# Kernel tuning notes

Hardware: AMD Instinct MI355X
Metric: run time of the kernel (lower is better)

The kernel has to match this reference:

```python
import jax, jax.numpy as jnp
import numpy as np

N, T, D, H = 32, 2048, 256, 256


def setup_inputs() -> dict:
    key = jax.random.key(0)
    k0, k1, k2, k3, k4 = jax.random.split(key, 5)
    std = 1.0 / np.sqrt(H + D)  # matches PTLSTM.reset()
    return {
        "x": jax.random.normal(k0, (N, T, D), dtype=jnp.float32),
        "state": jnp.zeros((N, 2 * H), dtype=jnp.float32),  # [h0 | c0]
        "w_ih": (jax.random.normal(k1, (4 * H, D)) * std).astype(jnp.float32),
        "w_hh": (jax.random.normal(k2, (4 * H, H)) * std).astype(jnp.float32),
        "b_ih": (jax.random.normal(k3, (4 * H,)) * std).astype(jnp.float32),
        "b_hh": (jax.random.normal(k4, (4 * H,)) * std).astype(jnp.float32),
    }


def reference(x, state, w_ih, w_hh, b_ih, b_hh):
    # Single-layer batch_first LSTM, PyTorch gate order (i, f, g, o).
    Hd = w_hh.shape[1]
    h0, c0 = state[:, :Hd], state[:, Hd:]
    # Precompute input-to-hidden projection for all timesteps (one big GEMM).
    xg = jnp.einsum('ntd,gd->ntg', x, w_ih) + (b_ih + b_hh)  # [N, T, 4H]

    def step(carry, xg_t):
        h, c = carry
        gates = xg_t + h @ w_hh.T  # [N, 4H]
        i, f, g, o = jnp.split(gates, 4, axis=-1)
        i = jax.nn.sigmoid(i)
        f = jax.nn.sigmoid(f)
        g = jnp.tanh(g)
        o = jax.nn.sigmoid(o)
        c = f * c + i * g
        h = o * jnp.tanh(c)
        return (h, c), h

    (hT, cT), out_t = jax.lax.scan(step, (h0, c0), jnp.swapaxes(xg, 0, 1))
    output = jnp.swapaxes(out_t, 0, 1)  # [N, T, H]
    outstate = jnp.concatenate([hT, cT], axis=1)  # [N, 2H]
    return output, outstate
```

## Files before the change

kernel.cpp:

```cpp
#include <hip/hip_runtime.h>

typedef _Float16 half2_t __attribute__((ext_vector_type(2)));
typedef __bf16   bf16x8  __attribute__((ext_vector_type(8)));
typedef float    f32x4   __attribute__((ext_vector_type(4)));
typedef unsigned short u16x8 __attribute__((ext_vector_type(8)));
typedef unsigned int  uint32;
typedef unsigned long long uint64;

#define LSTM_N 32
#define LSTM_T 2048
#define LSTM_D 256
#define LSTM_H 256
#define NG 1024
#define CH 256
#define NCH (LSTM_T / CH)
#define MCH (LSTM_N * CH)

#define OFF_XG   ((size_t)0)
#define SZ_XG    ((size_t)MCH * NG * 4)
#define OFF_WIHB (OFF_XG + SZ_XG)
#define SZ_WIHB  ((size_t)NG * LSTM_D * 2)
#define OFF_BIAS (OFF_WIHB + SZ_WIHB)
#define SZ_BIAS  ((size_t)4096)
#define OFF_WPK  (OFF_BIAS + SZ_BIAS)
#define SZ_WPK   ((size_t)2 * 512 * 128 * 4)
#define OFF_CST  (OFF_WPK + SZ_WPK)
#define SZ_CST   ((size_t)LSTM_N * 256 * 4)
#define OFF_HST  (OFF_CST + SZ_CST)
#define SZ_HST   ((size_t)LSTM_N * 128 * 4)
#define OFF_HX   (OFF_HST + SZ_HST)
#define SZ_HX    ((size_t)LSTM_N * 2 * 2 * 64 * 8)

#if defined(__has_builtin)
#if __has_builtin(__builtin_amdgcn_fdot2)
#define HAVE_FDOT2 1
#endif
#endif

__device__ __forceinline__ float fdot2(uint32 w, uint32 h, float acc) {
#ifdef HAVE_FDOT2
  return __builtin_amdgcn_fdot2(__builtin_bit_cast(half2_t, w),
                                __builtin_bit_cast(half2_t, h), acc, false);
#else
  half2_t wv = __builtin_bit_cast(half2_t, w);
  half2_t hv = __builtin_bit_cast(half2_t, h);
  float r = fmaf((float)wv.x, (float)hv.x, acc);
  return fmaf((float)wv.y, (float)hv.y, r);
#endif
}

__device__ __forceinline__ float sigm(float x) { return 1.f / (1.f + __expf(-x)); }
__device__ __forceinline__ float tanh_fast(float x) { return 2.f / (1.f + __expf(-2.f * x)) - 1.f; }

__device__ __forceinline__ unsigned short f2bf(float f) {
  uint32 u = __builtin_bit_cast(uint32, f);
  uint32 r = (u + 0x7FFFu + ((u >> 16) & 1u)) >> 16;
  return (unsigned short)r;
}

__device__ __forceinline__ float bfly8(const float a[8], int kap) {
  float k0[4], g0[4];
  const bool b4 = (kap & 4) != 0;
#pragma unroll
  for (int v = 0; v < 4; ++v) {
    k0[v] = b4 ? a[v + 4] : a[v];
    g0[v] = b4 ? a[v] : a[v + 4];
  }
#pragma unroll
  for (int v = 0; v < 4; ++v) k0[v] += __shfl_xor(g0[v], 4, 64);
  float k1[2], g1[2];
  const bool b2 = (kap & 2) != 0;
#pragma unroll
  for (int v = 0; v < 2; ++v) {
    k1[v] = b2 ? k0[v + 2] : k0[v];
    g1[v] = b2 ? k0[v] : k0[v + 2];
  }
#pragma unroll
  for (int v = 0; v < 2; ++v) k1[v] += __shfl_xor(g1[v], 2, 64);
  const bool b1 = (kap & 1) != 0;
  float k2 = b1 ? k1[1] : k1[0];
  float g2 = b1 ? k1[0] : k1[1];
  return k2 + __shfl_xor(g2, 1, 64);
}


__global__ void cvt_bf16_k(const float* __restrict__ src, unsigned short* __restrict__ dst, int n) {
  int i = blockIdx.x * blockDim.x + threadIdx.x;
  if (4 * i + 3 < n) {
    float4 v = ((const float4*)src)[i];
    ushort4 o;
    o.x = f2bf(v.x); o.y = f2bf(v.y); o.z = f2bf(v.z); o.w = f2bf(v.w);
    ((ushort4*)dst)[i] = o;
  }
}

__global__ void bias_sum_k(const float* __restrict__ bih, const float* __restrict__ bhh,
                           float* __restrict__ bias) {
  int g = blockIdx.x * blockDim.x + threadIdx.x;
  if (g < NG) bias[g] = bih[g] + bhh[g];
}

__global__ void wpack_k(const float* __restrict__ whh, uint32* __restrict__ wpk) {
  int e = blockIdx.x * blockDim.x + threadIdx.x;
  int p = e >> 16;
  int i128 = (e >> 9) & 127;
  int t = e & 511;
  int j = i128 >> 4, m = i128 & 15;
  int w = t >> 6, l = t & 63;
  int q = l >> 4, b3 = (l >> 3) & 1, kap = l & 7;
  int row = q * 256 + 128 * p + 16 * w + 8 * b3 + j;
  int k = (m < 8) ? (128 * p + 16 * kap + 2 * m)
                  : (128 * (1 - p) + 16 * kap + 2 * (m - 8));
  half2_t h;
  h.x = (_Float16)whh[row * 256 + k];
  h.y = (_Float16)whh[row * 256 + k + 1];
  wpk[((i128 >> 2) * 1024 + p * 512 + t) * 4 + (i128 & 3)] = __builtin_bit_cast(uint32, h);
}

__global__ void state_init_k(const float* __restrict__ state, float* __restrict__ cst,
                             uint32* __restrict__ hst, uint64* __restrict__ hx) {
  int i = blockIdx.x * blockDim.x + threadIdx.x;
  int n = i >> 8, j = i & 255;
  cst[i] = state[n * 512 + 256 + j];
  if ((j & 1) == 0) {
    half2_t h2;
    h2.x = (_Float16)state[n * 512 + j];
    h2.y = (_Float16)state[n * 512 + j + 1];
    hst[(n << 7) + (j >> 1)] = __builtin_bit_cast(uint32, h2);
  }
  hx[i] = 0ull;
}

__global__ __launch_bounds__(256) void gemm_xg(const float* __restrict__ x,
                                               const unsigned short* __restrict__ wb,
                                               const float* __restrict__ bias,
                                               float* __restrict__ xg, int ch) {
  __shared__ unsigned short As[128 * 40];
  __shared__ unsigned short Bs[128 * 40];
  const int tid = threadIdx.x;
  const int m0 = blockIdx.y * 128;
  const int g0 = blockIdx.x * 128;
  const int w = tid >> 6;
  const int lane = tid & 63;
  const int wm = (w >> 1) * 64, wn = (w & 1) * 64;
  const int row_l = tid >> 2;
  const int q = tid & 3;
  const int lr = lane & 15, kg = lane >> 4;

  size_t grow[2];
#pragma unroll
  for (int r = 0; r < 2; ++r) {
    int gm = m0 + row_l + 64 * r;
    grow[r] = (size_t)(gm >> 8) * LSTM_T + (size_t)ch * CH + (gm & 255);
  }

  f32x4 acc[4][4];
#pragma unroll
  for (int i = 0; i < 4; ++i)
#pragma unroll
    for (int j = 0; j < 4; ++j) acc[i][j] = (f32x4){0.f, 0.f, 0.f, 0.f};

  for (int kt = 0; kt < 8; ++kt) {
#pragma unroll
    for (int r = 0; r < 2; ++r) {
      int row = row_l + 64 * r;
      const float* ap = x + grow[r] * 256 + kt * 32 + q * 8;
      float4 v0 = *(const float4*)ap;
      float4 v1 = *(const float4*)(ap + 4);
      u16x8 o;
      o[0] = f2bf(v0.x); o[1] = f2bf(v0.y); o[2] = f2bf(v0.z); o[3] = f2bf(v0.w);
      o[4] = f2bf(v1.x); o[5] = f2bf(v1.y); o[6] = f2bf(v1.z); o[7] = f2bf(v1.w);
      *(uint4*)((char*)As + row * 80 + q * 16) = __builtin_bit_cast(uint4, o);
      uint4 bv = *(const uint4*)(wb + (size_t)(g0 + row) * 256 + kt * 32 + q * 8);
      *(uint4*)((char*)Bs + row * 80 + q * 16) = bv;
    }
    __syncthreads();
    bf16x8 af[4], bfr[4];
#pragma unroll
    for (int i = 0; i < 4; ++i)
      af[i] = __builtin_bit_cast(bf16x8, *(const uint4*)((char*)As + (wm + 16 * i + lr) * 80 + kg * 16));
#pragma unroll
    for (int j = 0; j < 4; ++j)
      bfr[j] = __builtin_bit_cast(bf16x8, *(const uint4*)((char*)Bs + (wn + 16 * j + lr) * 80 + kg * 16));
#pragma unroll
    for (int i = 0; i < 4; ++i)
#pragma unroll
      for (int j = 0; j < 4; ++j)
        acc[i][j] = __builtin_amdgcn_mfma_f32_16x16x32_bf16(af[i], bfr[j], acc[i][j], 0, 0, 0);
    __syncthreads();
  }
#pragma unroll
  for (int j = 0; j < 4; ++j) {
    int gc = g0 + wn + 16 * j + lr;
    float bj = bias[gc];
#pragma unroll
    for (int i = 0; i < 4; ++i) {
#pragma unroll
      for (int r = 0; r < 4; ++r) {
        int m = m0 + wm + 16 * i + kg * 4 + r;
        xg[(size_t)m * NG + gc] = acc[i][j][r] + bj;
      }
    }
  }
}

__global__ __launch_bounds__(512, 1) void lstm_scan(const float* __restrict__ xg,
                                                    const uint4* __restrict__ wpk4,
                                                    float* __restrict__ cst,
                                                    uint32* __restrict__ hst,
                                                    uint64* __restrict__ hx,
                                                    float* __restrict__ out, int ch) {
  __shared__ uint32 hown[2][64];
  __shared__ uint32 hpeer[64];
  __shared__ float ostage[16][128];

  const int b = blockIdx.x;
  const int n = b & 31;
  const int p = b >> 5;
  const int t = threadIdx.x;
  const int w = t >> 6, l = t & 63;
  const int q = l >> 4, kap = l & 7;
  const int u = 16 * w + (l & 15);
  const int R = q * 256 + 128 * p + u;

  uint32 wr[128];
#pragma unroll
  for (int ig = 0; ig < 32; ++ig) {
    uint4 v = wpk4[ig * 1024 + p * 512 + t];
    wr[4 * ig + 0] = v.x; wr[4 * ig + 1] = v.y; wr[4 * ig + 2] = v.z; wr[4 * ig + 3] = v.w;
  }
  float c = cst[n * 256 + 128 * p + u];
  if (t < 64) {
    hown[0][t] = hst[n * 128 + 64 * p + t];
    hpeer[t]   = hst[n * 128 + 64 * (1 - p) + t];
  }
  __syncthreads();

  const float* xgn = xg + (size_t)n * CH * NG;
  float* outb = out + ((size_t)n * LSTM_T + (size_t)ch * CH) * LSTM_H;
  uint64* hx_own  = hx + (size_t)(n * 2 + p) * 128;
  uint64* hx_peer = hx + (size_t)(n * 2 + (1 - p)) * 128;
  const int gsbase = ch * CH;

  float xcur = xgn[R];

  for (int tt = 0; tt < CH; ++tt) {
    const uint32 gs = (uint32)(gsbase + tt);
    float xnext = (tt < CH - 1) ? xgn[(size_t)(tt + 1) * NG + R] : 0.f;
    uint32 hro[8];
    *(uint4*)&hro[0] = *(const uint4*)&hown[tt & 1][8 * kap];
    *(uint4*)&hro[4] = *(const uint4*)&hown[tt & 1][8 * kap + 4];
    float acc[8];
#pragma unroll
    for (int j = 0; j < 8; ++j) {
      float a = 0.f;
#pragma unroll
      for (int m = 0; m < 8; ++m) a = fdot2(wr[j * 16 + m], hro[m], a);
      acc[j] = a;
    }
    if (tt > 0 && t < 64) {
      uint64 v;
      do {
        v = __hip_atomic_load(&hx_peer[(size_t)(tt & 1) * 64 + t],
                              __ATOMIC_RELAXED, __HIP_MEMORY_SCOPE_AGENT);
      } while ((uint32)(v >> 32) != gs);
      hpeer[t] = (uint32)v;
    }
    __syncthreads();
    uint32 hrp[8];
    *(uint4*)&hrp[0] = *(const uint4*)&hpeer[8 * kap];
    *(uint4*)&hrp[4] = *(const uint4*)&hpeer[8 * kap + 4];
#pragma unroll
    for (int j = 0; j < 8; ++j) {
      float a = acc[j];
#pragma unroll
      for (int m = 0; m < 8; ++m) a = fdot2(wr[j * 16 + 8 + m], hrp[m], a);
      acc[j] = a;
    }
    float s = bfly8(acc, kap);
    float pre = s + xcur;
    xcur = xnext;
    float z = (q == 2) ? (2.f * pre) : pre;
    float sg = 1.f / (1.f + __expf(-z));
    float a_own = (q == 2) ? (2.f * sg - 1.f) : sg;
    float a1 = __shfl_xor(a_own, 16, 64);
    float a2 = __shfl_xor(a_own, 32, 64);
    float a3 = __shfl_xor(a1, 32, 64);
    float gi = (q == 0) ? a_own : ((q == 1) ? a1 : ((q == 2) ? a2 : a3));
    float gf = (q == 1) ? a_own : ((q == 0) ? a1 : ((q == 3) ? a2 : a3));
    float gg = (q == 2) ? a_own : ((q == 3) ? a1 : ((q == 0) ? a2 : a3));
    float go = (q == 3) ? a_own : ((q == 2) ? a1 : ((q == 1) ? a2 : a3));
    c = gf * c + gi * gg;
    float h = go * tanh_fast(c);
    _Float16 hf16 = (_Float16)h;
    uint32 hz = (uint32)__builtin_bit_cast(unsigned short, hf16);
    uint32 hn = (uint32)__shfl_xor((int)hz, 1, 64);
    if (q == 0) {
      ((unsigned short*)&hown[(tt + 1) & 1][0])[u] = (unsigned short)hz;
      ostage[tt & 15][u] = h;
      if (tt < CH - 1 && (l & 1) == 0) {
        uint64 msg = (uint64)(hz | (hn << 16)) | ((uint64)(gs + 1) << 32);
        __hip_atomic_store(&hx_own[(size_t)((tt + 1) & 1) * 64 + (u >> 1)], msg,
                           __ATOMIC_RELAXED, __HIP_MEMORY_SCOPE_AGENT);
      }
      if (ch == NCH - 1 && tt == CH - 1) {
        float* os = out + (size_t)LSTM_N * LSTM_T * LSTM_H + n * 512;
        os[128 * p + u] = h;
        os[256 + 128 * p + u] = c;
      }
    }
    __syncthreads();
    if ((tt & 15) == 15) {
      int sl = t >> 5, q4 = t & 31;
      float4 v = *(const float4*)&ostage[sl][4 * q4];
      *(float4*)&outb[(size_t)(tt - 15 + sl) * LSTM_H + 128 * p + 4 * q4] = v;
    }
  }
  if (q == 0) cst[n * 256 + 128 * p + u] = c;
  if (t < 64) hst[n * 128 + 64 * p + t] = hown[0][t];
}

extern "C" void kernel_launch(void* const* d_in, const int* in_sizes, int n_in,
                              void* d_out, int out_size, void* d_ws, size_t ws_size,
                              hipStream_t stream) {
  const float* x   = (const float*)d_in[0];
  const float* st  = (const float*)d_in[1];
  const float* wih = (const float*)d_in[2];
  const float* whh = (const float*)d_in[3];
  const float* bih = (const float*)d_in[4];
  const float* bhh = (const float*)d_in[5];
  float* out = (float*)d_out;
  char* ws = (char*)d_ws;

  float* xg = (float*)(ws + OFF_XG);
  unsigned short* wihb = (unsigned short*)(ws + OFF_WIHB);
  float* bias = (float*)(ws + OFF_BIAS);
  uint32* wpk = (uint32*)(ws + OFF_WPK);
  float* cst = (float*)(ws + OFF_CST);
  uint32* hst = (uint32*)(ws + OFF_HST);
  uint64* hx = (uint64*)(ws + OFF_HX);

  cvt_bf16_k<<<(NG * LSTM_D / 4 + 255) / 256, 256, 0, stream>>>(wih, wihb, NG * LSTM_D);
  bias_sum_k<<<4, 256, 0, stream>>>(bih, bhh, bias);
  wpack_k<<<512, 256, 0, stream>>>(whh, wpk);
  state_init_k<<<32, 256, 0, stream>>>(st, cst, hst, hx);

  for (int ch = 0; ch < NCH; ++ch) {
    gemm_xg<<<dim3(NG / 128, MCH / 128), 256, 0, stream>>>(x, wihb, bias, xg, ch);
    lstm_scan<<<64, 512, 0, stream>>>(xg, (const uint4*)wpk, cst, hst, hx, out, ch);
  }
}
```

Before: 2.978 ms.

## Split recurrent matvec by K-halves and exchange partial gate sums instead of h

Each of the two blocks per sequence now multiplies all 1024 gate rows against only its own half of h, so no block waits for the peer's h before starting its matvec. Partial pre-activations for the peer's rows go through global memory slots tagged with a step counter. The owning block waits for them, applies the activations into shared memory, and updates the cell. This removes the bfly8 shuffle reduction and the mid-step wait on peer h. In exchange, each step sends 1024 64-bit messages per sequence instead of 64 and polls them with s_sleep.

```diff
diff --git a/kernel.cpp b/kernel.cpp
--- a/kernel.cpp
+++ b/kernel.cpp
@@ -28,8 +28,8 @@
 #define SZ_CST   ((size_t)LSTM_N * 256 * 4)
 #define OFF_HST  (OFF_CST + SZ_CST)
 #define SZ_HST   ((size_t)LSTM_N * 128 * 4)
-#define OFF_HX   (OFF_HST + SZ_HST)
-#define SZ_HX    ((size_t)LSTM_N * 2 * 2 * 64 * 8)
+#define OFF_HPX  (OFF_HST + SZ_HST)
+#define SZ_HPX   ((size_t)LSTM_N * 2 * 1024 * 8)
 
 #if defined(__has_builtin)
 #if __has_builtin(__builtin_amdgcn_fdot2)
@@ -58,31 +58,6 @@
   return (unsigned short)r;
 }
 
-__device__ __forceinline__ float bfly8(const float a[8], int kap) {
-  float k0[4], g0[4];
-  const bool b4 = (kap & 4) != 0;
-#pragma unroll
-  for (int v = 0; v < 4; ++v) {
-    k0[v] = b4 ? a[v + 4] : a[v];
-    g0[v] = b4 ? a[v] : a[v + 4];
-  }
-#pragma unroll
-  for (int v = 0; v < 4; ++v) k0[v] += __shfl_xor(g0[v], 4, 64);
-  float k1[2], g1[2];
-  const bool b2 = (kap & 2) != 0;
-#pragma unroll
-  for (int v = 0; v < 2; ++v) {
-    k1[v] = b2 ? k0[v + 2] : k0[v];
-    g1[v] = b2 ? k0[v] : k0[v + 2];
-  }
-#pragma unroll
-  for (int v = 0; v < 2; ++v) k1[v] += __shfl_xor(g1[v], 2, 64);
-  const bool b1 = (kap & 1) != 0;
-  float k2 = b1 ? k1[1] : k1[0];
-  float g2 = b1 ? k1[0] : k1[1];
-  return k2 + __shfl_xor(g2, 1, 64);
-}
-
 
 __global__ void cvt_bf16_k(const float* __restrict__ src, unsigned short* __restrict__ dst, int n) {
   int i = blockIdx.x * blockDim.x + threadIdx.x;
@@ -103,22 +78,19 @@
 __global__ void wpack_k(const float* __restrict__ whh, uint32* __restrict__ wpk) {
   int e = blockIdx.x * blockDim.x + threadIdx.x;
   int p = e >> 16;
-  int i128 = (e >> 9) & 127;
+  int i = (e >> 9) & 127;
   int t = e & 511;
-  int j = i128 >> 4, m = i128 & 15;
-  int w = t >> 6, l = t & 63;
-  int q = l >> 4, b3 = (l >> 3) & 1, kap = l & 7;
-  int row = q * 256 + 128 * p + 16 * w + 8 * b3 + j;
-  int k = (m < 8) ? (128 * p + 16 * kap + 2 * m)
-                  : (128 * (1 - p) + 16 * kap + 2 * (m - 8));
+  int rh = i >> 6, jj = i & 63;
+  int row = t + rh * 512;
+  int k = 128 * p + 2 * jj;
   half2_t h;
   h.x = (_Float16)whh[row * 256 + k];
   h.y = (_Float16)whh[row * 256 + k + 1];
-  wpk[((i128 >> 2) * 1024 + p * 512 + t) * 4 + (i128 & 3)] = __builtin_bit_cast(uint32, h);
+  wpk[((i >> 2) * 1024 + p * 512 + t) * 4 + (i & 3)] = __builtin_bit_cast(uint32, h);
 }
 
 __global__ void state_init_k(const float* __restrict__ state, float* __restrict__ cst,
-                             uint32* __restrict__ hst, uint64* __restrict__ hx) {
+                             uint32* __restrict__ hst, uint64* __restrict__ hpx) {
   int i = blockIdx.x * blockDim.x + threadIdx.x;
   int n = i >> 8, j = i & 255;
   cst[i] = state[n * 512 + 256 + j];
@@ -128,7 +100,8 @@
     h2.y = (_Float16)state[n * 512 + j + 1];
     hst[(n << 7) + (j >> 1)] = __builtin_bit_cast(uint32, h2);
   }
-  hx[i] = 0ull;
+#pragma unroll
+  for (int z = 0; z < 8; ++z) hpx[(size_t)i * 8 + z] = 0ull;
 }
 
 __global__ __launch_bounds__(256) void gemm_xg(const float* __restrict__ x,
@@ -208,101 +181,105 @@
                                                     const uint4* __restrict__ wpk4,
                                                     float* __restrict__ cst,
                                                     uint32* __restrict__ hst,
-                                                    uint64* __restrict__ hx,
+                                                    uint64* __restrict__ hpx,
                                                     float* __restrict__ out, int ch) {
+  __shared__ float actb[512];
   __shared__ uint32 hown[2][64];
-  __shared__ uint32 hpeer[64];
   __shared__ float ostage[16][128];
 
   const int b = blockIdx.x;
   const int n = b & 31;
   const int p = b >> 5;
   const int t = threadIdx.x;
-  const int w = t >> 6, l = t & 63;
-  const int q = l >> 4, kap = l & 7;
-  const int u = 16 * w + (l & 15);
-  const int R = q * 256 + 128 * p + u;
+  const int q1 = t >> 8;
+  const int v = t & 255;
+  const int u = v & 127;
+  const bool own = ((v >> 7) == p);
+  const bool iscell = own && (q1 == 0);
+  const int r1 = t, r2 = t + 512;
 
   uint32 wr[128];
 #pragma unroll
   for (int ig = 0; ig < 32; ++ig) {
-    uint4 v = wpk4[ig * 1024 + p * 512 + t];
-    wr[4 * ig + 0] = v.x; wr[4 * ig + 1] = v.y; wr[4 * ig + 2] = v.z; wr[4 * ig + 3] = v.w;
-  }
-  float c = cst[n * 256 + 128 * p + u];
-  if (t < 64) {
-    hown[0][t] = hst[n * 128 + 64 * p + t];
-    hpeer[t]   = hst[n * 128 + 64 * (1 - p) + t];
-  }
+    uint4 w4 = wpk4[ig * 1024 + p * 512 + t];
+    wr[4 * ig + 0] = w4.x; wr[4 * ig + 1] = w4.y; wr[4 * ig + 2] = w4.z; wr[4 * ig + 3] = w4.w;
+  }
+  float c = 0.f;
+  if (iscell) c = cst[n * 256 + 128 * p + u];
+  if (t < 64) hown[0][t] = hst[n * 128 + 64 * p + t];
   __syncthreads();
 
   const float* xgn = xg + (size_t)n * CH * NG;
   float* outb = out + ((size_t)n * LSTM_T + (size_t)ch * CH) * LSTM_H;
-  uint64* hx_own  = hx + (size_t)(n * 2 + p) * 128;
-  uint64* hx_peer = hx + (size_t)(n * 2 + (1 - p)) * 128;
+  uint64* slots = hpx + (size_t)n * 2048;
   const int gsbase = ch * CH;
 
-  float xcur = xgn[R];
+  float x1 = 0.f, x2 = 0.f;
+  if (own) { x1 = xgn[r1]; x2 = xgn[r2]; }
 
   for (int tt = 0; tt < CH; ++tt) {
-    const uint32 gs = (uint32)(gsbase + tt);
-    float xnext = (tt < CH - 1) ? xgn[(size_t)(tt + 1) * NG + R] : 0.f;
-    uint32 hro[8];
-    *(uint4*)&hro[0] = *(const uint4*)&hown[tt & 1][8 * kap];
-    *(uint4*)&hro[4] = *(const uint4*)&hown[tt & 1][8 * kap + 4];
-    float acc[8];
-#pragma unroll
-    for (int j = 0; j < 8; ++j) {
-      float a = 0.f;
-#pragma unroll
-      for (int m = 0; m < 8; ++m) a = fdot2(wr[j * 16 + m], hro[m], a);
-      acc[j] = a;
-    }
-    if (tt > 0 && t < 64) {
-      uint64 v;
-      do {
-        v = __hip_atomic_load(&hx_peer[(size_t)(tt & 1) * 64 + t],
-                              __ATOMIC_RELAXED, __HIP_MEMORY_SCOPE_AGENT);
-      } while ((uint32)(v >> 32) != gs);
-      hpeer[t] = (uint32)v;
+    const uint32 want = (uint32)(gsbase + tt) + 1;
+    const int par = tt & 1;
+    float a1 = 0.f, a2 = 0.f;
+    const uint32* hp = &hown[par][0];
+#pragma unroll
+    for (int c4 = 0; c4 < 4; ++c4) {
+      uint32 hh[16];
+      *(uint4*)&hh[0]  = *(const uint4*)&hp[16 * c4 + 0];
+      *(uint4*)&hh[4]  = *(const uint4*)&hp[16 * c4 + 4];
+      *(uint4*)&hh[8]  = *(const uint4*)&hp[16 * c4 + 8];
+      *(uint4*)&hh[12] = *(const uint4*)&hp[16 * c4 + 12];
+      float s1 = 0.f, s2 = 0.f;
+#pragma unroll
+      for (int j = 0; j < 16; ++j) {
+        s1 = fdot2(wr[16 * c4 + j],      hh[j], s1);
+        s2 = fdot2(wr[64 + 16 * c4 + j], hh[j], s2);
+      }
+      a1 += s1; a2 += s2;
+    }
+    if (own) {
+      uint64 m1, m2;
+      uint64* s1p = &slots[(size_t)par * 1024 + r1];
+      uint64* s2p = &slots[(size_t)par * 1024 + r2];
+      for (;;) {
+        m1 = __hip_atomic_load(s1p, __ATOMIC_RELAXED, __HIP_MEMORY_SCOPE_AGENT);
+        if ((uint32)(m1 >> 32) == want) break;
+        __builtin_amdgcn_s_sleep(1);
+      }
+      for (;;) {
+        m2 = __hip_atomic_load(s2p, __ATOMIC_RELAXED, __HIP_MEMORY_SCOPE_AGENT);
+        if ((uint32)(m2 >> 32) == want) break;
+        __builtin_amdgcn_s_sleep(1);
+      }
+      float pre1 = a1 + __builtin_bit_cast(float, (uint32)m1) + x1;
+      float pre2 = a2 + __builtin_bit_cast(float, (uint32)m2) + x2;
+      if (tt < CH - 1) {
+        x1 = xgn[(size_t)(tt + 1) * NG + r1];
+        x2 = xgn[(size_t)(tt + 1) * NG + r2];
+      }
+      float g1 = sigm(pre1);
+      float g2 = (q1 == 0) ? tanh_fast(pre2) : sigm(pre2);
+      actb[q1 * 128 + u] = g1;
+      actb[(q1 + 2) * 128 + u] = g2;
+    } else {
+      __hip_atomic_store(&slots[(size_t)par * 1024 + r1],
+                         (uint64)__builtin_bit_cast(uint32, a1) | ((uint64)want << 32),
+                         __ATOMIC_RELAXED, __HIP_MEMORY_SCOPE_AGENT);
+      __hip_atomic_store(&slots[(size_t)par * 1024 + r2],
+                         (uint64)__builtin_bit_cast(uint32, a2) | ((uint64)want << 32),
+                         __ATOMIC_RELAXED, __HIP_MEMORY_SCOPE_AGENT);
     }
     __syncthreads();
-    uint32 hrp[8];
-    *(uint4*)&hrp[0] = *(const uint4*)&hpeer[8 * kap];
-    *(uint4*)&hrp[4] = *(const uint4*)&hpeer[8 * kap + 4];
-#pragma unroll
-    for (int j = 0; j < 8; ++j) {
-      float a = acc[j];
-#pragma unroll
-      for (int m = 0; m < 8; ++m) a = fdot2(wr[j * 16 + 8 + m], hrp[m], a);
-      acc[j] = a;
-    }
-    float s = bfly8(acc, kap);
-    float pre = s + xcur;
-    xcur = xnext;
-    float z = (q == 2) ? (2.f * pre) : pre;
-    float sg = 1.f / (1.f + __expf(-z));
-    float a_own = (q == 2) ? (2.f * sg - 1.f) : sg;
-    float a1 = __shfl_xor(a_own, 16, 64);
-    float a2 = __shfl_xor(a_own, 32, 64);
-    float a3 = __shfl_xor(a1, 32, 64);
-    float gi = (q == 0) ? a_own : ((q == 1) ? a1 : ((q == 2) ? a2 : a3));
-    float gf = (q == 1) ? a_own : ((q == 0) ? a1 : ((q == 3) ? a2 : a3));
-    float gg = (q == 2) ? a_own : ((q == 3) ? a1 : ((q == 0) ? a2 : a3));
-    float go = (q == 3) ? a_own : ((q == 2) ? a1 : ((q == 1) ? a2 : a3));
-    c = gf * c + gi * gg;
-    float h = go * tanh_fast(c);
-    _Float16 hf16 = (_Float16)h;
-    uint32 hz = (uint32)__builtin_bit_cast(unsigned short, hf16);
-    uint32 hn = (uint32)__shfl_xor((int)hz, 1, 64);
-    if (q == 0) {
-      ((unsigned short*)&hown[(tt + 1) & 1][0])[u] = (unsigned short)hz;
+    if (iscell) {
+      float gi = actb[u];
+      float gf = actb[128 + u];
+      float gg = actb[256 + u];
+      float go = actb[384 + u];
+      c = gf * c + gi * gg;
+      float h = go * tanh_fast(c);
+      _Float16 hf = (_Float16)h;
+      ((unsigned short*)&hown[par ^ 1][0])[u] = __builtin_bit_cast(unsigned short, hf);
       ostage[tt & 15][u] = h;
-      if (tt < CH - 1 && (l & 1) == 0) {
-        uint64 msg = (uint64)(hz | (hn << 16)) | ((uint64)(gs + 1) << 32);
-        __hip_atomic_store(&hx_own[(size_t)((tt + 1) & 1) * 64 + (u >> 1)], msg,
-                           __ATOMIC_RELAXED, __HIP_MEMORY_SCOPE_AGENT);
-      }
       if (ch == NCH - 1 && tt == CH - 1) {
         float* os = out + (size_t)LSTM_N * LSTM_T * LSTM_H + n * 512;
         os[128 * p + u] = h;
@@ -312,11 +289,11 @@
     __syncthreads();
     if ((tt & 15) == 15) {
       int sl = t >> 5, q4 = t & 31;
-      float4 v = *(const float4*)&ostage[sl][4 * q4];
-      *(float4*)&outb[(size_t)(tt - 15 + sl) * LSTM_H + 128 * p + 4 * q4] = v;
-    }
-  }
-  if (q == 0) cst[n * 256 + 128 * p + u] = c;
+      float4 vv = *(const float4*)&ostage[sl][4 * q4];
+      *(float4*)&outb[(size_t)(tt - 15 + sl) * LSTM_H + 128 * p + 4 * q4] = vv;
+    }
+  }
+  if (iscell) cst[n * 256 + 128 * p + u] = c;
   if (t < 64) hst[n * 128 + 64 * p + t] = hown[0][t];
 }
 
@@ -338,15 +315,15 @@
   uint32* wpk = (uint32*)(ws + OFF_WPK);
   float* cst = (float*)(ws + OFF_CST);
   uint32* hst = (uint32*)(ws + OFF_HST);
-  uint64* hx = (uint64*)(ws + OFF_HX);
+  uint64* hpx = (uint64*)(ws + OFF_HPX);
 
   cvt_bf16_k<<<(NG * LSTM_D / 4 + 255) / 256, 256, 0, stream>>>(wih, wihb, NG * LSTM_D);
   bias_sum_k<<<4, 256, 0, stream>>>(bih, bhh, bias);
   wpack_k<<<512, 256, 0, stream>>>(whh, wpk);
-  state_init_k<<<32, 256, 0, stream>>>(st, cst, hst, hx);
+  state_init_k<<<32, 256, 0, stream>>>(st, cst, hst, hpx);
 
   for (int ch = 0; ch < NCH; ++ch) {
     gemm_xg<<<dim3(NG / 128, MCH / 128), 256, 0, stream>>>(x, wihb, bias, xg, ch);
-    lstm_scan<<<64, 512, 0, stream>>>(xg, (const uint4*)wpk, cst, hst, hx, out, ch);
-  }
-}
+    lstm_scan<<<64, 512, 0, stream>>>(xg, (const uint4*)wpk, cst, hst, hpx, out, ch);
+  }
+}
```

Measured after the change: 4.142 ms. 39.1% more time.

## Interleave two batch rows per scan block to hide peer h-exchange latency

Applied to the files above, without the earlier changes.

Each lstm_scan block now processes two batch rows (n and n+16) back to back within every timestep. Each row has its own shared h buffers, cell state and cross-block handshake, and the grid shrinks from 64 to 32 blocks. The aim is to hide the spin-wait on the peer block's hidden-state message for one row behind the recurrent matvec of the other row. It also drops one barrier per row-step. The cost is twice the serial work per block and fewer active CUs, so the critical path may simply get longer if the exchange latency is not the dominant cost.

```diff
diff --git a/kernel.cpp b/kernel.cpp
--- a/kernel.cpp
+++ b/kernel.cpp
@@ -49,7 +49,6 @@
 #endif
 }
 
-__device__ __forceinline__ float sigm(float x) { return 1.f / (1.f + __expf(-x)); }
 __device__ __forceinline__ float tanh_fast(float x) { return 2.f / (1.f + __expf(-2.f * x)) - 1.f; }
 
 __device__ __forceinline__ unsigned short f2bf(float f) {
@@ -210,13 +209,14 @@
                                                     uint32* __restrict__ hst,
                                                     uint64* __restrict__ hx,
                                                     float* __restrict__ out, int ch) {
-  __shared__ uint32 hown[2][64];
-  __shared__ uint32 hpeer[64];
-  __shared__ float ostage[16][128];
+  __shared__ uint32 hownA[2][64], hownB[2][64];
+  __shared__ uint32 hpeerA[64], hpeerB[64];
+  __shared__ float ostage[2][16][128];
 
   const int b = blockIdx.x;
-  const int n = b & 31;
-  const int p = b >> 5;
+  const int n = b & 15;
+  const int p = b >> 4;
+  const int nA = n, nB = n + 16;
   const int t = threadIdx.x;
   const int w = t >> 6, l = t & 63;
   const int q = l >> 4, kap = l & 7;
@@ -229,95 +229,179 @@
     uint4 v = wpk4[ig * 1024 + p * 512 + t];
     wr[4 * ig + 0] = v.x; wr[4 * ig + 1] = v.y; wr[4 * ig + 2] = v.z; wr[4 * ig + 3] = v.w;
   }
-  float c = cst[n * 256 + 128 * p + u];
+  float cA = cst[nA * 256 + 128 * p + u];
+  float cB = cst[nB * 256 + 128 * p + u];
   if (t < 64) {
-    hown[0][t] = hst[n * 128 + 64 * p + t];
-    hpeer[t]   = hst[n * 128 + 64 * (1 - p) + t];
+    hownA[0][t] = hst[nA * 128 + 64 * p + t];
+    hpeerA[t]   = hst[nA * 128 + 64 * (1 - p) + t];
+    hownB[0][t] = hst[nB * 128 + 64 * p + t];
+    hpeerB[t]   = hst[nB * 128 + 64 * (1 - p) + t];
   }
   __syncthreads();
 
-  const float* xgn = xg + (size_t)n * CH * NG;
-  float* outb = out + ((size_t)n * LSTM_T + (size_t)ch * CH) * LSTM_H;
-  uint64* hx_own  = hx + (size_t)(n * 2 + p) * 128;
-  uint64* hx_peer = hx + (size_t)(n * 2 + (1 - p)) * 128;
+  const float* xgA = xg + (size_t)nA * CH * NG;
+  const float* xgB = xg + (size_t)nB * CH * NG;
+  float* outA = out + ((size_t)nA * LSTM_T + (size_t)ch * CH) * LSTM_H;
+  float* outB = out + ((size_t)nB * LSTM_T + (size_t)ch * CH) * LSTM_H;
+  uint64* hxA_own  = hx + (size_t)(nA * 2 + p) * 128;
+  uint64* hxA_peer = hx + (size_t)(nA * 2 + (1 - p)) * 128;
+  uint64* hxB_own  = hx + (size_t)(nB * 2 + p) * 128;
+  uint64* hxB_peer = hx + (size_t)(nB * 2 + (1 - p)) * 128;
   const int gsbase = ch * CH;
 
-  float xcur = xgn[R];
+  float xcA = xgA[R];
+  float xcB = xgB[R];
 
   for (int tt = 0; tt < CH; ++tt) {
     const uint32 gs = (uint32)(gsbase + tt);
-    float xnext = (tt < CH - 1) ? xgn[(size_t)(tt + 1) * NG + R] : 0.f;
-    uint32 hro[8];
-    *(uint4*)&hro[0] = *(const uint4*)&hown[tt & 1][8 * kap];
-    *(uint4*)&hro[4] = *(const uint4*)&hown[tt & 1][8 * kap + 4];
-    float acc[8];
-#pragma unroll
-    for (int j = 0; j < 8; ++j) {
-      float a = 0.f;
-#pragma unroll
-      for (int m = 0; m < 8; ++m) a = fdot2(wr[j * 16 + m], hro[m], a);
-      acc[j] = a;
+    {
+      float xnext = (tt < CH - 1) ? xgA[(size_t)(tt + 1) * NG + R] : 0.f;
+      uint32 hro[8];
+      *(uint4*)&hro[0] = *(const uint4*)&hownA[tt & 1][8 * kap];
+      *(uint4*)&hro[4] = *(const uint4*)&hownA[tt & 1][8 * kap + 4];
+      float acc[8];
+#pragma unroll
+      for (int j = 0; j < 8; ++j) {
+        float a = 0.f;
+#pragma unroll
+        for (int m = 0; m < 8; ++m) a = fdot2(wr[j * 16 + m], hro[m], a);
+        acc[j] = a;
+      }
+      if (tt > 0 && t < 64) {
+        uint64 v;
+        do {
+          v = __hip_atomic_load(&hxA_peer[(size_t)(tt & 1) * 64 + t],
+                                __ATOMIC_RELAXED, __HIP_MEMORY_SCOPE_AGENT);
+        } while ((uint32)(v >> 32) != gs);
+        hpeerA[t] = (uint32)v;
+      }
+      __syncthreads();
+      uint32 hrp[8];
+      *(uint4*)&hrp[0] = *(const uint4*)&hpeerA[8 * kap];
+      *(uint4*)&hrp[4] = *(const uint4*)&hpeerA[8 * kap + 4];
+#pragma unroll
+      for (int j = 0; j < 8; ++j) {
+        float a = acc[j];
+#pragma unroll
+        for (int m = 0; m < 8; ++m) a = fdot2(wr[j * 16 + 8 + m], hrp[m], a);
+        acc[j] = a;
+      }
+      float s = bfly8(acc, kap);
+      float pre = s + xcA;
+      xcA = xnext;
+      float z = (q == 2) ? (2.f * pre) : pre;
+      float sg = 1.f / (1.f + __expf(-z));
+      float a_own = (q == 2) ? (2.f * sg - 1.f) : sg;
+      float a1 = __shfl_xor(a_own, 16, 64);
+      float a2 = __shfl_xor(a_own, 32, 64);
+      float a3 = __shfl_xor(a1, 32, 64);
+      float gi = (q == 0) ? a_own : ((q == 1) ? a1 : ((q == 2) ? a2 : a3));
+      float gf = (q == 1) ? a_own : ((q == 0) ? a1 : ((q == 3) ? a2 : a3));
+      float gg = (q == 2) ? a_own : ((q == 3) ? a1 : ((q == 0) ? a2 : a3));
+      float go = (q == 3) ? a_own : ((q == 2) ? a1 : ((q == 1) ? a2 : a3));
+      cA = gf * cA + gi * gg;
+      float h = go * tanh_fast(cA);
+      _Float16 hf16 = (_Float16)h;
+      uint32 hz = (uint32)__builtin_bit_cast(unsigned short, hf16);
+      uint32 hn = (uint32)__shfl_xor((int)hz, 1, 64);
+      if (q == 0) {
+        ((unsigned short*)&hownA[(tt + 1) & 1][0])[u] = (unsigned short)hz;
+        ostage[0][tt & 15][u] = h;
+        if (tt < CH - 1 && (l & 1) == 0) {
+          uint64 msg = (uint64)(hz | (hn << 16)) | ((uint64)(gs + 1) << 32);
+          __hip_atomic_store(&hxA_own[(size_t)((tt + 1) & 1) * 64 + (u >> 1)], msg,
+                             __ATOMIC_RELAXED, __HIP_MEMORY_SCOPE_AGENT);
+        }
+        if (ch == NCH - 1 && tt == CH - 1) {
+          float* os = out + (size_t)LSTM_N * LSTM_T * LSTM_H + nA * 512;
+          os[128 * p + u] = h;
+          os[256 + 128 * p + u] = cA;
+        }
+      }
     }
-    if (tt > 0 && t < 64) {
-      uint64 v;
-      do {
-        v = __hip_atomic_load(&hx_peer[(size_t)(tt & 1) * 64 + t],
-                              __ATOMIC_RELAXED, __HIP_MEMORY_SCOPE_AGENT);
-      } while ((uint32)(v >> 32) != gs);
-      hpeer[t] = (uint32)v;
+    {
+      float xnext = (tt < CH - 1) ? xgB[(size_t)(tt + 1) * NG + R] : 0.f;
+      uint32 hro[8];
+      *(uint4*)&hro[0] = *(const uint4*)&hownB[tt & 1][8 * kap];
+      *(uint4*)&hro[4] = *(const uint4*)&hownB[tt & 1][8 * kap + 4];
+      float acc[8];
+#pragma unroll
+      for (int j = 0; j < 8; ++j) {
+        float a = 0.f;
+#pragma unroll
+        for (int m = 0; m < 8; ++m) a = fdot2(wr[j * 16 + m], hro[m], a);
+        acc[j] = a;
+      }
+      if (tt > 0 && t >= 64 && t < 128) {
+        int sl = t - 64;
+        uint64 v;
+        do {
+          v = __hip_atomic_load(&hxB_peer[(size_t)(tt & 1) * 64 + sl],
+                                __ATOMIC_RELAXED, __HIP_MEMORY_SCOPE_AGENT);
+        } while ((uint32)(v >> 32) != gs);
+        hpeerB[sl] = (uint32)v;
+      }
+      __syncthreads();
+      uint32 hrp[8];
+      *(uint4*)&hrp[0] = *(const uint4*)&hpeerB[8 * kap];
+      *(uint4*)&hrp[4] = *(const uint4*)&hpeerB[8 * kap + 4];
+#pragma unroll
+      for (int j = 0; j < 8; ++j) {
+        float a = acc[j];
+#pragma unroll
+        for (int m = 0; m < 8; ++m) a = fdot2(wr[j * 16 + 8 + m], hrp[m], a);
+        acc[j] = a;
+      }
+      float s = bfly8(acc, kap);
+      float pre = s + xcB;
+      xcB = xnext;
+      float z = (q == 2) ? (2.f * pre) : pre;
+      float sg = 1.f / (1.f + __expf(-z));
+      float a_own = (q == 2) ? (2.f * sg - 1.f) : sg;
+      float a1 = __shfl_xor(a_own, 16, 64);
+      float a2 = __shfl_xor(a_own, 32, 64);
+      float a3 = __shfl_xor(a1, 32, 64);
+      float gi = (q == 0) ? a_own : ((q == 1) ? a1 : ((q == 2) ? a2 : a3));
+      float gf = (q == 1) ? a_own : ((q == 0) ? a1 : ((q == 3) ? a2 : a3));
+      float gg = (q == 2) ? a_own : ((q == 3) ? a1 : ((q == 0) ? a2 : a3));
+      float go = (q == 3) ? a_own : ((q == 2) ? a1 : ((q == 1) ? a2 : a3));
+      cB = gf * cB + gi * gg;
+      float h = go * tanh_fast(cB);
+      _Float16 hf16 = (_Float16)h;
+      uint32 hz = (uint32)__builtin_bit_cast(unsigned short, hf16);
+      uint32 hn = (uint32)__shfl_xor((int)hz, 1, 64);
+      if (q == 0) {
+        ((unsigned short*)&hownB[(tt + 1) & 1][0])[u] = (unsigned short)hz;
+        ostage[1][tt & 15][u] = h;
+        if (tt < CH - 1 && (l & 1) == 0) {
+          uint64 msg = (uint64)(hz | (hn << 16)) | ((uint64)(gs + 1) << 32);
+          __hip_atomic_store(&hxB_own[(size_t)((tt + 1) & 1) * 64 + (u >> 1)], msg,
+                             __ATOMIC_RELAXED, __HIP_MEMORY_SCOPE_AGENT);
+        }
+        if (ch == NCH - 1 && tt == CH - 1) {
+          float* os = out + (size_t)LSTM_N * LSTM_T * LSTM_H + nB * 512;
+          os[128 * p + u] = h;
+          os[256 + 128 * p + u] = cB;
+        }
+      }
     }
-    __syncthreads();
-    uint32 hrp[8];
-    *(uint4*)&hrp[0] = *(const uint4*)&hpeer[8 * kap];
-    *(uint4*)&hrp[4] = *(const uint4*)&hpeer[8 * kap + 4];
-#pragma unroll
-    for (int j = 0; j < 8; ++j) {
-      float a = acc[j];
-#pragma unroll
-      for (int m = 0; m < 8; ++m) a = fdot2(wr[j * 16 + 8 + m], hrp[m], a);
-      acc[j] = a;
+    if ((tt & 15) == 15) {
+      __syncthreads();
+      int sl = t >> 5, g4 = t & 31;
+      float4 vA = *(const float4*)&ostage[0][sl][4 * g4];
+      *(float4*)&outA[(size_t)(tt - 15 + sl) * LSTM_H + 128 * p + 4 * g4] = vA;
+      float4 vB = *(const float4*)&ostage[1][sl][4 * g4];
+      *(float4*)&outB[(size_t)(tt - 15 + sl) * LSTM_H + 128 * p + 4 * g4] = vB;
     }
-    float s = bfly8(acc, kap);
-    float pre = s + xcur;
-    xcur = xnext;
-    float z = (q == 2) ? (2.f * pre) : pre;
-    float sg = 1.f / (1.f + __expf(-z));
-    float a_own = (q == 2) ? (2.f * sg - 1.f) : sg;
-    float a1 = __shfl_xor(a_own, 16, 64);
-    float a2 = __shfl_xor(a_own, 32, 64);
-    float a3 = __shfl_xor(a1, 32, 64);
-    float gi = (q == 0) ? a_own : ((q == 1) ? a1 : ((q == 2) ? a2 : a3));
-    float gf = (q == 1) ? a_own : ((q == 0) ? a1 : ((q == 3) ? a2 : a3));
-    float gg = (q == 2) ? a_own : ((q == 3) ? a1 : ((q == 0) ? a2 : a3));
-    float go = (q == 3) ? a_own : ((q == 2) ? a1 : ((q == 1) ? a2 : a3));
-    c = gf * c + gi * gg;
-    float h = go * tanh_fast(c);
-    _Float16 hf16 = (_Float16)h;
-    uint32 hz = (uint32)__builtin_bit_cast(unsigned short, hf16);
-    uint32 hn = (uint32)__shfl_xor((int)hz, 1, 64);
-    if (q == 0) {
-      ((unsigned short*)&hown[(tt + 1) & 1][0])[u] = (unsigned short)hz;
-      ostage[tt & 15][u] = h;
-      if (tt < CH - 1 && (l & 1) == 0) {
-        uint64 msg = (uint64)(hz | (hn << 16)) | ((uint64)(gs + 1) << 32);
-        __hip_atomic_store(&hx_own[(size_t)((tt + 1) & 1) * 64 + (u >> 1)], msg,
-                           __ATOMIC_RELAXED, __HIP_MEMORY_SCOPE_AGENT);
-      }
-      if (ch == NCH - 1 && tt == CH - 1) {
-        float* os = out + (size_t)LSTM_N * LSTM_T * LSTM_H + n * 512;
-        os[128 * p + u] = h;
-        os[256 + 128 * p + u] = c;
-      }
-    }
-    __syncthreads();
-    if ((tt & 15) == 15) {
-      int sl = t >> 5, q4 = t & 31;
-      float4 v = *(const float4*)&ostage[sl][4 * q4];
-      *(float4*)&outb[(size_t)(tt - 15 + sl) * LSTM_H + 128 * p + 4 * q4] = v;
-    }
-  }
-  if (q == 0) cst[n * 256 + 128 * p + u] = c;
-  if (t < 64) hst[n * 128 + 64 * p + t] = hown[0][t];
+  }
+  if (q == 0) {
+    cst[nA * 256 + 128 * p + u] = cA;
+    cst[nB * 256 + 128 * p + u] = cB;
+  }
+  if (t < 64) {
+    hst[nA * 128 + 64 * p + t] = hownA[0][t];
+    hst[nB * 128 + 64 * p + t] = hownB[0][t];
+  }
 }
 
 extern "C" void kernel_launch(void* const* d_in, const int* in_sizes, int n_in,
@@ -347,6 +431,6 @@
 
   for (int ch = 0; ch < NCH; ++ch) {
     gemm_xg<<<dim3(NG / 128, MCH / 128), 256, 0, stream>>>(x, wihb, bias, xg, ch);
-    lstm_scan<<<64, 512, 0, stream>>>(xg, (const uint4*)wpk, cst, hst, hx, out, ch);
-  }
-}
+    lstm_scan<<<32, 512, 0, stream>>>(xg, (const uint4*)wpk, cst, hst, hx, out, ch);
+  }
+}
```

After: 4.604 ms. 1.55x slower.
